# Optimization experiments

Hardware: AMD Instinct MI355X
Metric: run time of the kernel (lower is better)

## Reference

```python
import jax, jax.numpy as jnp
import numpy as np

N = 20000      # nodes
E = 320000     # edges (before self loops)
D_IN = 256
D_H = 256
D_E = 8
NEG_SLOPE = 0.2


def setup_inputs() -> dict:
    key = jax.random.key(0)
    ks = jax.random.split(key, 12)
    x = jax.random.normal(ks[0], (N, D_IN), jnp.float32)
    edge_index = jax.random.randint(ks[1], (2, E), 0, N, dtype=jnp.int32)
    edge_attr = jax.random.normal(ks[2], (E, D_E), jnp.float32)
    batch = jnp.zeros((N,), jnp.int32)

    def gat_params(k, d_in):
        k1, k2, k3 = jax.random.split(k, 3)
        W = jax.random.normal(k1, (d_in, D_H), jnp.float32) * (1.0 / np.sqrt(d_in))
        a_s = jax.random.normal(k2, (D_H,), jnp.float32) * 0.1
        a_d = jax.random.normal(k3, (D_H,), jnp.float32) * 0.1
        b = jnp.zeros((D_H,), jnp.float32)
        return W, a_s, a_d, b

    W1, as1, ad1, b1 = gat_params(ks[3], D_IN)
    W2, as2, ad2, b2 = gat_params(ks[4], D_H)
    W3, as3, ad3, b3 = gat_params(ks[5], D_H)
    return dict(x=x, edge_index=edge_index, edge_attr=edge_attr, batch=batch,
                W1=W1, as1=as1, ad1=ad1, b1=b1,
                W2=W2, as2=as2, ad2=ad2, b2=b2,
                W3=W3, as3=as3, ad3=ad3, b3=b3)


def gat_conv(x, src, dst, W, a_src, a_dst, b):
    # PyG GATConv, heads=1: h = x W; alpha_e = leakyrelu(<h_src,a_s> + <h_dst,a_d>)
    h = x @ W                                  # [N, D_H]
    s = h @ a_src                              # [N]
    d = h @ a_dst                              # [N]
    alpha = jax.nn.leaky_relu(s[src] + d[dst], NEG_SLOPE)   # [Etot]
    n = h.shape[0]
    m = jax.ops.segment_max(alpha, dst, num_segments=n)     # per-dst max
    ex = jnp.exp(alpha - m[dst])
    denom = jax.ops.segment_sum(ex, dst, num_segments=n)
    w = ex / (denom[dst] + 1e-16)
    out = jax.ops.segment_sum(h[src] * w[:, None], dst, num_segments=n)
    return out + b


def reference(x, edge_index, edge_attr, batch,
              W1, as1, ad1, b1, W2, as2, ad2, b2, W3, as3, ad3, b3):
    # row-normalize input features (zero norms -> 1e-8)
    norms = jnp.linalg.norm(x, axis=1, keepdims=True)
    norms = jnp.where(norms == 0, 1e-8, norms)
    x = x / norms

    # add self loops once (GATConv default add_self_loops=True);
    # edge_attr is ignored since edge_dim=None in GATConv defaults.
    loop = jnp.arange(N, dtype=edge_index.dtype)
    src = jnp.concatenate([edge_index[0], loop])
    dst = jnp.concatenate([edge_index[1], loop])

    x = jax.nn.gelu(gat_conv(x, src, dst, W1, as1, ad1, b1), approximate=False)
    x = jax.nn.gelu(gat_conv(x, src, dst, W2, as2, ad2, b2), approximate=False)
    x = jax.nn.gelu(gat_conv(x, src, dst, W3, as3, ad3, b3), approximate=False)
    return x
```

## Files before the change

### kernel.cpp

```cpp
#include <hip/hip_runtime.h>
#include <math.h>

#define NN 20000
#define EE 320000
#define DD 256
#define ETOT (EE + NN)
#define EDGE_CAP 1536

typedef __attribute__((ext_vector_type(8))) short bf8;
typedef __attribute__((ext_vector_type(4))) float f32x4;

__device__ __forceinline__ float gelu_exact(float x) {
    return 0.5f * x * (1.0f + erff(x * 0.70710678118654752f));
}

__device__ __forceinline__ unsigned short f2bf(float v) {
    unsigned u = __float_as_uint(v);
    u += 0x7fffu + ((u >> 16) & 1u);
    return (unsigned short)(u >> 16);
}
__device__ __forceinline__ float bf2f(unsigned short h) {
    return __uint_as_float(((unsigned)h) << 16);
}
__device__ __forceinline__ void split2(float v, unsigned short& hi, unsigned short& lo) {
    hi = f2bf(v);
    lo = f2bf(v - bf2f(hi));
}

__global__ __launch_bounds__(256) void norm_k(const float* __restrict__ X,
                                              unsigned short* __restrict__ Xh,
                                              unsigned short* __restrict__ Xl,
                                              float* __restrict__ sdZero,
                                              int* __restrict__ deg) {
    int t = threadIdx.x;
    int bid = blockIdx.x;
    if (t < 24) sdZero[bid * 24 + t] = 0.0f;
    if (t >= 32 && t < 36) deg[bid * 4 + (t - 32)] = 1;

    int wave = (bid * 256 + t) >> 6;
    int lane = t & 63;
    const float4 v = *(const float4*)&X[wave * DD + lane * 4];
    float ss = v.x * v.x + v.y * v.y + v.z * v.z + v.w * v.w;
    for (int off = 32; off > 0; off >>= 1) ss += __shfl_down(ss, off, 64);
    ss = __shfl(ss, 0, 64);
    float n = sqrtf(ss);
    if (n == 0.0f) n = 1e-8f;
    float inv = 1.0f / n;
    float o[4] = {v.x * inv, v.y * inv, v.z * inv, v.w * inv};
    ushort4 hv, lv;
    split2(o[0], hv.x, lv.x);
    split2(o[1], hv.y, lv.y);
    split2(o[2], hv.z, lv.z);
    split2(o[3], hv.w, lv.w);
    *(ushort4*)&Xh[wave * DD + lane * 4] = hv;
    *(ushort4*)&Xl[wave * DD + lane * 4] = lv;
}

__global__ __launch_bounds__(256) void splitw_k(const float* __restrict__ W1, const float* __restrict__ W2,
                                                const float* __restrict__ W3, unsigned short* __restrict__ Whl) {
    __shared__ float tile[64][65];
    int t = threadIdx.x;
    int k0 = blockIdx.x * 64;
    int c0 = blockIdx.y * 64;
    int z = blockIdx.z;
    const float* W = (z == 0) ? W1 : (z == 1) ? W2 : W3;
    unsigned short* Wht = Whl + (size_t)z * 2 * DD * DD;
    unsigned short* Wlt = Wht + DD * DD;
#pragma unroll
    for (int i = 0; i < 16; ++i) {
        int idx = t + i * 256;
        int r = idx >> 6, c = idx & 63;
        tile[r][c] = W[(k0 + r) * DD + c0 + c];
    }
    __syncthreads();
#pragma unroll
    for (int i = 0; i < 16; ++i) {
        int idx = t + i * 256;
        int r = idx >> 6, c = idx & 63;
        float v = tile[c][r];
        unsigned short hi, lo;
        split2(v, hi, lo);
        Wht[(c0 + r) * DD + k0 + c] = hi;
        Wlt[(c0 + r) * DD + k0 + c] = lo;
    }
}

__global__ void count_k(const int* __restrict__ ei, int* deg) {
    int e = blockIdx.x * 256 + threadIdx.x;
    if (e < EE) atomicAdd(&deg[ei[EE + e]], 1);
}

#define SCAN_T 1024
#define ITEMS 20
__global__ __launch_bounds__(SCAN_T) void scan_k(const int* __restrict__ deg, int* __restrict__ offs,
                                                 int* __restrict__ cursor, int* __restrict__ csr) {
    __shared__ int part[SCAN_T];
    int t = threadIdx.x;
    int base = t * ITEMS;
    int local[ITEMS];
    int sum = 0;
#pragma unroll
    for (int i = 0; i < ITEMS; ++i) {
        int idx = base + i;
        int v = (idx < NN) ? deg[idx] : 0;
        local[i] = v;
        sum += v;
    }
    part[t] = sum;
    __syncthreads();
    for (int s = 1; s < SCAN_T; s <<= 1) {
        int v = (t >= s) ? part[t - s] : 0;
        __syncthreads();
        part[t] += v;
        __syncthreads();
    }
    int run = (t == 0) ? 0 : part[t - 1];
#pragma unroll
    for (int i = 0; i < ITEMS; ++i) {
        int idx = base + i;
        if (idx < NN) {
            offs[idx] = run;
            cursor[idx] = run + 1;
            csr[run] = idx;
            run += local[i];
        }
    }
    if (t == SCAN_T - 1) offs[NN] = part[SCAN_T - 1];
}

__global__ void fill_k(const int* __restrict__ ei, int* cursor, int* __restrict__ csr) {
    int e = blockIdx.x * 256 + threadIdx.x;
    if (e < EE) {
        int s = ei[e];
        int d = ei[EE + e];
        int p = atomicAdd(&cursor[d], 1);
        csr[p] = s;
    }
}

#define LDB 40
__global__ __launch_bounds__(256) void gemm_sd(const unsigned short* __restrict__ Xh,
                                               const unsigned short* __restrict__ Xl,
                                               const unsigned short* __restrict__ Bh,
                                               const unsigned short* __restrict__ Bl,
                                               const float* __restrict__ a_s,
                                               const float* __restrict__ a_d,
                                               float* __restrict__ H,
                                               float* __restrict__ sArr,
                                               float* __restrict__ dArr) {
    __shared__ unsigned short sBh[128 * LDB], sBl[128 * LDB];
    int t = threadIdx.x;
    int m0 = blockIdx.x * 64;
    int n0 = blockIdx.y * 128;
    int w = t >> 6, l = t & 63;
    int rofs = l & 15, kch = l >> 4;

    f32x4 acc[8] = {};

    int c1 = t, c2 = t + 256;
    int br1 = c1 >> 2, bo1 = (c1 & 3) * 8;
    int br2 = c2 >> 2, bo2 = (c2 & 3) * 8;
    const unsigned short* Bh1 = &Bh[(n0 + br1) * DD + bo1];
    const unsigned short* Bh2 = &Bh[(n0 + br2) * DD + bo2];
    const unsigned short* Bl1 = &Bl[(n0 + br1) * DD + bo1];
    const unsigned short* Bl2 = &Bl[(n0 + br2) * DD + bo2];
    bf8 rbh1 = *(const bf8*)Bh1;
    bf8 rbh2 = *(const bf8*)Bh2;
    bf8 rbl1 = *(const bf8*)Bl1;
    bf8 rbl2 = *(const bf8*)Bl2;

    int arow = m0 + w * 16 + rofs;
    bool aval = arow < NN;
    const unsigned short* Ahp = &Xh[(size_t)arow * DD + kch * 8];
    const unsigned short* Alp = &Xl[(size_t)arow * DD + kch * 8];
    bf8 zero = {0, 0, 0, 0, 0, 0, 0, 0};
    bf8 ah = aval ? *(const bf8*)Ahp : zero;
    bf8 al = aval ? *(const bf8*)Alp : zero;

    for (int k0 = 0; k0 < DD; k0 += 32) {
        if (k0) __syncthreads();
        *(bf8*)&sBh[br1 * LDB + bo1] = rbh1;
        *(bf8*)&sBh[br2 * LDB + bo2] = rbh2;
        *(bf8*)&sBl[br1 * LDB + bo1] = rbl1;
        *(bf8*)&sBl[br2 * LDB + bo2] = rbl2;
        __syncthreads();
        int kn = k0 + 32;
        bf8 nah = zero, nal = zero;
        if (kn < DD) {
            rbh1 = *(const bf8*)(Bh1 + kn);
            rbh2 = *(const bf8*)(Bh2 + kn);
            rbl1 = *(const bf8*)(Bl1 + kn);
            rbl2 = *(const bf8*)(Bl2 + kn);
            if (aval) {
                nah = *(const bf8*)(Ahp + kn);
                nal = *(const bf8*)(Alp + kn);
            }
        }
#pragma unroll
        for (int nt = 0; nt < 8; ++nt) {
            int r = nt * 16 + rofs;
            bf8 bh = *(const bf8*)&sBh[r * LDB + kch * 8];
            bf8 bl = *(const bf8*)&sBl[r * LDB + kch * 8];
            acc[nt] = __builtin_amdgcn_mfma_f32_16x16x32_bf16(ah, bh, acc[nt], 0, 0, 0);
            acc[nt] = __builtin_amdgcn_mfma_f32_16x16x32_bf16(ah, bl, acc[nt], 0, 0, 0);
            acc[nt] = __builtin_amdgcn_mfma_f32_16x16x32_bf16(al, bh, acc[nt], 0, 0, 0);
        }
        ah = nah;
        al = nal;
    }
    int row0 = m0 + w * 16 + (l >> 4) * 4;
    int colb = l & 15;
    float sp[4] = {0, 0, 0, 0}, dp[4] = {0, 0, 0, 0};
#pragma unroll
    for (int nt = 0; nt < 8; ++nt) {
        int cc = n0 + nt * 16 + colb;
        float vas = a_s[cc], vad = a_d[cc];
#pragma unroll
        for (int r = 0; r < 4; ++r) {
            int row = row0 + r;
            if (row < NN) H[(size_t)row * DD + cc] = acc[nt][r];
            sp[r] += acc[nt][r] * vas;
            dp[r] += acc[nt][r] * vad;
        }
    }
#pragma unroll
    for (int m = 1; m < 16; m <<= 1) {
#pragma unroll
        for (int r = 0; r < 4; ++r) {
            sp[r] += __shfl_xor(sp[r], m, 64);
            dp[r] += __shfl_xor(dp[r], m, 64);
        }
    }
    if (colb == 0) {
#pragma unroll
        for (int r = 0; r < 4; ++r) {
            int row = row0 + r;
            if (row < NN) {
                atomicAdd(&sArr[row], sp[r]);
                atomicAdd(&dArr[row], dp[r]);
            }
        }
    }
}

__global__ __launch_bounds__(256) void spmm_k(const float* __restrict__ H, const float* __restrict__ sArr,
                                              const float* __restrict__ dArr, const int* __restrict__ offs,
                                              const int* __restrict__ csr, const float* __restrict__ bias,
                                              unsigned short* __restrict__ Oh,
                                              unsigned short* __restrict__ Ol,
                                              float* __restrict__ outf32) {
    __shared__ float wLds[EDGE_CAP];
    __shared__ int sLds[EDGE_CAP];
    int t = threadIdx.x;
    int sub = t & 7;
    int g = t >> 3;
    int dst0 = blockIdx.y * 32;
    int dst = dst0 + g;
    int dim = blockIdx.x * 32 + sub * 4;

    int blkBeg = offs[dst0];
    int beg = offs[dst], end = offs[dst + 1];
    float dd = dArr[dst];

    float den = 0.0f;
    for (int e = beg + sub; e < end; e += 8) {
        int s = csr[e];
        float a = sArr[s] + dd;
        a = (a > 0.0f) ? a : 0.2f * a;
        float wv = expf(a);
        wLds[e - blkBeg] = wv;
        sLds[e - blkBeg] = s;
        den += wv;
    }
    den += __shfl_xor(den, 1, 64);
    den += __shfl_xor(den, 2, 64);
    den += __shfl_xor(den, 4, 64);
    float inv = 1.0f / den;
    for (int e = beg + sub; e < end; e += 8) wLds[e - blkBeg] *= inv;
    __syncthreads();

    const float* Hs = H + dim;
    float4 A0 = make_float4(0, 0, 0, 0), A1 = A0, A2 = A0, A3 = A0;
    int e = beg - blkBeg, lend = end - blkBeg;
    for (; e + 3 < lend; e += 4) {
        int s0 = sLds[e], s1 = sLds[e + 1], s2 = sLds[e + 2], s3 = sLds[e + 3];
        float w0 = wLds[e], w1 = wLds[e + 1], w2 = wLds[e + 2], w3 = wLds[e + 3];
        const float4 h0 = *(const float4*)&Hs[(size_t)s0 * DD];
        const float4 h1 = *(const float4*)&Hs[(size_t)s1 * DD];
        const float4 h2 = *(const float4*)&Hs[(size_t)s2 * DD];
        const float4 h3 = *(const float4*)&Hs[(size_t)s3 * DD];
        A0.x += w0 * h0.x; A0.y += w0 * h0.y; A0.z += w0 * h0.z; A0.w += w0 * h0.w;
        A1.x += w1 * h1.x; A1.y += w1 * h1.y; A1.z += w1 * h1.z; A1.w += w1 * h1.w;
        A2.x += w2 * h2.x; A2.y += w2 * h2.y; A2.z += w2 * h2.z; A2.w += w2 * h2.w;
        A3.x += w3 * h3.x; A3.y += w3 * h3.y; A3.z += w3 * h3.z; A3.w += w3 * h3.w;
    }
    for (; e < lend; ++e) {
        int s0 = sLds[e];
        float w0 = wLds[e];
        const float4 h0 = *(const float4*)&Hs[(size_t)s0 * DD];
        A0.x += w0 * h0.x; A0.y += w0 * h0.y; A0.z += w0 * h0.z; A0.w += w0 * h0.w;
    }

    const float4 b = *(const float4*)&bias[dim];
    float o0 = gelu_exact(A0.x + A1.x + A2.x + A3.x + b.x);
    float o1 = gelu_exact(A0.y + A1.y + A2.y + A3.y + b.y);
    float o2 = gelu_exact(A0.z + A1.z + A2.z + A3.z + b.z);
    float o3 = gelu_exact(A0.w + A1.w + A2.w + A3.w + b.w);

    ushort4 hv, lv;
    split2(o0, hv.x, lv.x);
    split2(o1, hv.y, lv.y);
    split2(o2, hv.z, lv.z);
    split2(o3, hv.w, lv.w);
    *(ushort4*)&Oh[dst * DD + dim] = hv;
    *(ushort4*)&Ol[dst * DD + dim] = lv;
    if (outf32) {
        float4 o = make_float4(o0, o1, o2, o3);
        *(float4*)&outf32[dst * DD + dim] = o;
    }
}

extern "C" void kernel_launch(void* const* d_in, const int* in_sizes, int n_in,
                              void* d_out, int out_size, void* d_ws, size_t ws_size,
                              hipStream_t stream) {
    const float* x  = (const float*)d_in[0];
    const int* ei   = (const int*)d_in[1];
    const float* W1 = (const float*)d_in[4];
    const float* as1 = (const float*)d_in[5];
    const float* ad1 = (const float*)d_in[6];
    const float* b1 = (const float*)d_in[7];
    const float* W2 = (const float*)d_in[8];
    const float* as2 = (const float*)d_in[9];
    const float* ad2 = (const float*)d_in[10];
    const float* b2 = (const float*)d_in[11];
    const float* W3 = (const float*)d_in[12];
    const float* as3 = (const float*)d_in[13];
    const float* ad3 = (const float*)d_in[14];
    const float* b3 = (const float*)d_in[15];

    float* H = (float*)d_ws;
    unsigned short* Xh = (unsigned short*)(H + (size_t)NN * DD);
    unsigned short* Xl = Xh + (size_t)NN * DD;
    unsigned short* Whl = Xl + (size_t)NN * DD;
    float* sd = (float*)(Whl + (size_t)6 * DD * DD);
    int* offs = (int*)(sd + (size_t)6 * NN);
    int* cursor = offs + (NN + 1);
    int* csr = cursor + NN;
    int* deg = csr + ETOT;

    float* sA1 = sd,           *dA1 = sd + NN;
    float* sA2 = sd + 2 * NN,  *dA2 = sd + 3 * NN;
    float* sA3 = sd + 4 * NN,  *dA3 = sd + 5 * NN;
    unsigned short* Wt1 = Whl;
    unsigned short* Wt2 = Whl + (size_t)2 * DD * DD;
    unsigned short* Wt3 = Whl + (size_t)4 * DD * DD;

    norm_k<<<NN / 4, 256, 0, stream>>>(x, Xh, Xl, sd, deg);
    count_k<<<(EE + 255) / 256, 256, 0, stream>>>(ei, deg);
    scan_k<<<1, SCAN_T, 0, stream>>>(deg, offs, cursor, csr);
    fill_k<<<(EE + 255) / 256, 256, 0, stream>>>(ei, cursor, csr);
    splitw_k<<<dim3(4, 4, 3), 256, 0, stream>>>(W1, W2, W3, Whl);

    dim3 ggrid((NN + 63) / 64, DD / 128);
    dim3 sgrid(DD / 32, NN / 32);

    gemm_sd<<<ggrid, 256, 0, stream>>>(Xh, Xl, Wt1, Wt1 + DD * DD, as1, ad1, H, sA1, dA1);
    spmm_k<<<sgrid, 256, 0, stream>>>(H, sA1, dA1, offs, csr, b1, Xh, Xl, nullptr);
    gemm_sd<<<ggrid, 256, 0, stream>>>(Xh, Xl, Wt2, Wt2 + DD * DD, as2, ad2, H, sA2, dA2);
    spmm_k<<<sgrid, 256, 0, stream>>>(H, sA2, dA2, offs, csr, b2, Xh, Xl, nullptr);
    gemm_sd<<<ggrid, 256, 0, stream>>>(Xh, Xl, Wt3, Wt3 + DD * DD, as3, ad3, H, sA3, dA3);
    spmm_k<<<sgrid, 256, 0, stream>>>(H, sA3, dA3, offs, csr, b3, Xh, Xl, (float*)d_out);
}
```

Measured before the change: 340.8 us.

## Restructure GAT aggregation to one wave per destination with edge-parallel shuffle reduction

The SpMM aggregation kernel now assigns one wavefront per destination node and splits each wave into 8 edge slots by 8 dimension chunks, instead of 8 threads per destination working through edges serially. Attention weights are computed and applied in a single pass. Per-slot partial sums and the softmax denominator are combined with cross-lane shuffles, and normalisation happens once at the end. This removes the LDS staging, the second normalisation pass and the block barrier, and exposes more independent gathers per destination. In exchange it adds shuffle reductions, and only one eighth of the lanes do the final writes.

```diff
diff --git a/kernel.cpp b/kernel.cpp
--- a/kernel.cpp
+++ b/kernel.cpp
@@ -5,7 +5,6 @@
 #define EE 320000
 #define DD 256
 #define ETOT (EE + NN)
-#define EDGE_CAP 1536
 
 typedef __attribute__((ext_vector_type(8))) short bf8;
 typedef __attribute__((ext_vector_type(4))) float f32x4;
@@ -249,74 +248,58 @@
                                               unsigned short* __restrict__ Oh,
                                               unsigned short* __restrict__ Ol,
                                               float* __restrict__ outf32) {
-    __shared__ float wLds[EDGE_CAP];
-    __shared__ int sLds[EDGE_CAP];
-    int t = threadIdx.x;
-    int sub = t & 7;
-    int g = t >> 3;
-    int dst0 = blockIdx.y * 32;
-    int dst = dst0 + g;
-    int dim = blockIdx.x * 32 + sub * 4;
-
-    int blkBeg = offs[dst0];
+    int t = threadIdx.x;
+    int l = t & 63;
+    int wv = t >> 6;
+    int chunk = l & 7;
+    int eslot = l >> 3;
+    int dst = blockIdx.y * 4 + wv;
+    int dim = blockIdx.x * 32 + chunk * 4;
+
     int beg = offs[dst], end = offs[dst + 1];
     float dd = dArr[dst];
-
+    const float* Hs = H + dim;
+
+    float4 acc = make_float4(0, 0, 0, 0);
     float den = 0.0f;
-    for (int e = beg + sub; e < end; e += 8) {
+    for (int e = beg + eslot; e < end; e += 8) {
         int s = csr[e];
         float a = sArr[s] + dd;
         a = (a > 0.0f) ? a : 0.2f * a;
-        float wv = expf(a);
-        wLds[e - blkBeg] = wv;
-        sLds[e - blkBeg] = s;
-        den += wv;
-    }
-    den += __shfl_xor(den, 1, 64);
-    den += __shfl_xor(den, 2, 64);
-    den += __shfl_xor(den, 4, 64);
-    float inv = 1.0f / den;
-    for (int e = beg + sub; e < end; e += 8) wLds[e - blkBeg] *= inv;
-    __syncthreads();
-
-    const float* Hs = H + dim;
-    float4 A0 = make_float4(0, 0, 0, 0), A1 = A0, A2 = A0, A3 = A0;
-    int e = beg - blkBeg, lend = end - blkBeg;
-    for (; e + 3 < lend; e += 4) {
-        int s0 = sLds[e], s1 = sLds[e + 1], s2 = sLds[e + 2], s3 = sLds[e + 3];
-        float w0 = wLds[e], w1 = wLds[e + 1], w2 = wLds[e + 2], w3 = wLds[e + 3];
-        const float4 h0 = *(const float4*)&Hs[(size_t)s0 * DD];
-        const float4 h1 = *(const float4*)&Hs[(size_t)s1 * DD];
-        const float4 h2 = *(const float4*)&Hs[(size_t)s2 * DD];
-        const float4 h3 = *(const float4*)&Hs[(size_t)s3 * DD];
-        A0.x += w0 * h0.x; A0.y += w0 * h0.y; A0.z += w0 * h0.z; A0.w += w0 * h0.w;
-        A1.x += w1 * h1.x; A1.y += w1 * h1.y; A1.z += w1 * h1.z; A1.w += w1 * h1.w;
-        A2.x += w2 * h2.x; A2.y += w2 * h2.y; A2.z += w2 * h2.z; A2.w += w2 * h2.w;
-        A3.x += w3 * h3.x; A3.y += w3 * h3.y; A3.z += w3 * h3.z; A3.w += w3 * h3.w;
-    }
-    for (; e < lend; ++e) {
-        int s0 = sLds[e];
-        float w0 = wLds[e];
-        const float4 h0 = *(const float4*)&Hs[(size_t)s0 * DD];
-        A0.x += w0 * h0.x; A0.y += w0 * h0.y; A0.z += w0 * h0.z; A0.w += w0 * h0.w;
-    }
-
-    const float4 b = *(const float4*)&bias[dim];
-    float o0 = gelu_exact(A0.x + A1.x + A2.x + A3.x + b.x);
-    float o1 = gelu_exact(A0.y + A1.y + A2.y + A3.y + b.y);
-    float o2 = gelu_exact(A0.z + A1.z + A2.z + A3.z + b.z);
-    float o3 = gelu_exact(A0.w + A1.w + A2.w + A3.w + b.w);
-
-    ushort4 hv, lv;
-    split2(o0, hv.x, lv.x);
-    split2(o1, hv.y, lv.y);
-    split2(o2, hv.z, lv.z);
-    split2(o3, hv.w, lv.w);
-    *(ushort4*)&Oh[dst * DD + dim] = hv;
-    *(ushort4*)&Ol[dst * DD + dim] = lv;
-    if (outf32) {
-        float4 o = make_float4(o0, o1, o2, o3);
-        *(float4*)&outf32[dst * DD + dim] = o;
+        float w = expf(a);
+        den += w;
+        const float4 h = *(const float4*)&Hs[(size_t)s * DD];
+        acc.x += w * h.x;
+        acc.y += w * h.y;
+        acc.z += w * h.z;
+        acc.w += w * h.w;
+    }
+#pragma unroll
+    for (int m = 8; m < 64; m <<= 1) {
+        acc.x += __shfl_xor(acc.x, m, 64);
+        acc.y += __shfl_xor(acc.y, m, 64);
+        acc.z += __shfl_xor(acc.z, m, 64);
+        acc.w += __shfl_xor(acc.w, m, 64);
+        den += __shfl_xor(den, m, 64);
+    }
+    if (eslot == 0) {
+        float inv = 1.0f / den;
+        const float4 b = *(const float4*)&bias[dim];
+        float o0 = gelu_exact(acc.x * inv + b.x);
+        float o1 = gelu_exact(acc.y * inv + b.y);
+        float o2 = gelu_exact(acc.z * inv + b.z);
+        float o3 = gelu_exact(acc.w * inv + b.w);
+        ushort4 hv, lv;
+        split2(o0, hv.x, lv.x);
+        split2(o1, hv.y, lv.y);
+        split2(o2, hv.z, lv.z);
+        split2(o3, hv.w, lv.w);
+        *(ushort4*)&Oh[dst * DD + dim] = hv;
+        *(ushort4*)&Ol[dst * DD + dim] = lv;
+        if (outf32) {
+            float4 o = make_float4(o0, o1, o2, o3);
+            *(float4*)&outf32[dst * DD + dim] = o;
+        }
     }
 }
 
@@ -362,7 +345,7 @@
     splitw_k<<<dim3(4, 4, 3), 256, 0, stream>>>(W1, W2, W3, Whl);
 
     dim3 ggrid((NN + 63) / 64, DD / 128);
-    dim3 sgrid(DD / 32, NN / 32);
+    dim3 sgrid(DD / 32, NN / 4);
 
     gemm_sd<<<ggrid, 256, 0, stream>>>(Xh, Xl, Wt1, Wt1 + DD * DD, as1, ad1, H, sA1, dA1);
     spmm_k<<<sgrid, 256, 0, stream>>>(H, sA1, dA1, offs, csr, b1, Xh, Xl, nullptr);
```

Result: slower. 429.1 us (+25.9%).
